# Kernel optimization log

Measured on AMD Instinct MI355X. Metric: run time of the kernel, lower is better.

Reference implementation:

```python
import jax, jax.numpy as jnp
import numpy as np
from jax import lax

MAX_INT = 10000.0
V, T0, E, H = 100000, 20, 256, 256
T = T0 + 2          # tagset_size + 2 (start = T-2, stop = T-1)
B, S = 32, 512
H2 = H // 2


def setup_inputs() -> dict:
    key = jax.random.key(0)
    ks = jax.random.split(key, 18)
    sd = 0.08
    trans = jax.random.normal(ks[0], (T, T), jnp.float32)
    trans = trans.at[-2, :].set(-MAX_INT).at[:, -1].set(-MAX_INT)
    return {
        "X": jax.random.randint(ks[1], (B, S), 0, V, jnp.int64),
        "Y": jax.random.randint(ks[2], (B, S), 0, T0, jnp.int64),
        "emb": jax.random.normal(ks[3], (V, E), jnp.float32) * sd,
        "Wih_f": jax.random.normal(ks[4], (4 * H2, E), jnp.float32) * sd,
        "Whh_f": jax.random.normal(ks[5], (4 * H2, H2), jnp.float32) * sd,
        "bih_f": jax.random.normal(ks[6], (4 * H2,), jnp.float32) * sd,
        "bhh_f": jax.random.normal(ks[7], (4 * H2,), jnp.float32) * sd,
        "Wih_b": jax.random.normal(ks[8], (4 * H2, E), jnp.float32) * sd,
        "Whh_b": jax.random.normal(ks[9], (4 * H2, H2), jnp.float32) * sd,
        "bih_b": jax.random.normal(ks[10], (4 * H2,), jnp.float32) * sd,
        "bhh_b": jax.random.normal(ks[11], (4 * H2,), jnp.float32) * sd,
        "fcW": jax.random.normal(ks[12], (T, H), jnp.float32) * sd,
        "fcb": jax.random.normal(ks[13], (T,), jnp.float32) * sd,
        "trans": trans,
        # original draws random (h0, c0) of shape (2, seq_len, H//2) each call
        "h0": jax.random.normal(ks[14], (2, S, H2), jnp.float32),
        "c0": jax.random.normal(ks[15], (2, S, H2), jnp.float32),
    }


def _lstm_dir(x, h0, c0, Wih, Whh, bih, bhh, reverse):
    # x: [B, S, E]; scans over axis 0 (as torch LSTM with batch_first=False does here)
    def step(carry, xt):
        h, c = carry
        g = xt @ Wih.T + bih + h @ Whh.T + bhh          # [S, 4*H2]
        i, f, gg, o = jnp.split(g, 4, axis=-1)
        c2 = jax.nn.sigmoid(f) * c + jax.nn.sigmoid(i) * jnp.tanh(gg)
        h2 = jax.nn.sigmoid(o) * jnp.tanh(c2)
        return (h2, c2), h2
    xs = x[::-1] if reverse else x
    _, hs = lax.scan(step, (h0, c0), xs)
    return hs[::-1] if reverse else hs                  # [B, S, H2]


def _feats(X, emb, Wih_f, Whh_f, bih_f, bhh_f, Wih_b, Whh_b, bih_b, bhh_b,
           fcW, fcb, h0, c0):
    e = emb[X]                                           # [B, S, E]
    hf = _lstm_dir(e, h0[0], c0[0], Wih_f, Whh_f, bih_f, bhh_f, False)
    hb = _lstm_dir(e, h0[1], c0[1], Wih_b, Whh_b, bih_b, bhh_b, True)
    lstm_out = jnp.concatenate([hf, hb], axis=-1)        # [B, S, H]
    return lstm_out @ fcW.T + fcb                        # [B, S, T]


def _crf_loss(feats, Y, trans):
    # forward algorithm (log partition), vectorized over batch
    alpha0 = jnp.full((B, T), -MAX_INT, feats.dtype).at[:, -2].set(0.0)

    def step(alpha, feat_t):                             # feat_t: [B, T]
        # alpha_new[b, next] = LSE_prev(alpha[b,prev] + trans[next,prev]) + feat[b,next]
        new = jax.nn.logsumexp(alpha[:, None, :] + trans[None, :, :], axis=2) + feat_t
        return new, None

    alpha, _ = lax.scan(step, alpha0, jnp.swapaxes(feats, 0, 1))
    forward_score = jax.nn.logsumexp(alpha + trans[-1][None, :], axis=1).mean()

    # gold score
    start = jnp.full((B, 1), T - 2, Y.dtype)
    tags = jnp.concatenate([start, Y], axis=1)           # [B, S+1]
    emit = jnp.take_along_axis(feats, Y[..., None], axis=2)[..., 0].sum(axis=1)
    trans_sc = trans[tags[:, 1:], tags[:, :-1]].sum(axis=1) + trans[-1, tags[:, -1]]
    gold_score = (emit + trans_sc).mean()
    return forward_score - gold_score


def reference(X, Y, emb, Wih_f, Whh_f, bih_f, bhh_f, Wih_b, Whh_b, bih_b, bhh_b,
              fcW, fcb, trans, h0, c0):
    feats = _feats(X, emb, Wih_f, Whh_f, bih_f, bhh_f, Wih_b, Whh_b, bih_b, bhh_b,
                   fcW, fcb, h0, c0)
    score = _crf_loss(feats, Y, trans)
    return score, Y
```

## Files before the change

kernel.cpp:

```cpp
#include <hip/hip_runtime.h>
#include <hip/hip_bf16.h>
#include <stdint.h>

typedef __attribute__((ext_vector_type(8))) short short8;
typedef __attribute__((ext_vector_type(4))) float f32x4;
typedef __attribute__((ext_vector_type(4))) unsigned short ushort4v;

#define NB 32
#define NS 512
#define NE 256
#define NH2 128
#define NG 512
#define NT 22

__device__ __forceinline__ unsigned short f2bf(float f) {
    union { float f; unsigned u; } v; v.f = f;
    unsigned r = v.u + 0x7fffu + ((v.u >> 16) & 1u);
    return (unsigned short)(r >> 16);
}
__device__ __forceinline__ float bf2f(unsigned short b) {
    union { unsigned u; float f; } v; v.u = ((unsigned)b) << 16;
    return v.f;
}
__device__ __forceinline__ float sigmoidf_(float x) {
    return __builtin_amdgcn_rcpf(1.f + __expf(-x));
}
__device__ __forceinline__ float tanhf_(float x) {
    return 1.f - 2.f * __builtin_amdgcn_rcpf(__expf(2.f * x) + 1.f);
}
__device__ __forceinline__ void wg_barrier() {
    __builtin_amdgcn_sched_barrier(0);
    asm volatile("s_waitcnt lgkmcnt(0)" ::: "memory");
    __builtin_amdgcn_s_barrier();
    __builtin_amdgcn_sched_barrier(0);
}
#define GL16(gsrc, ldst)                                                              \
    __builtin_amdgcn_global_load_lds(                                                 \
        (const __attribute__((address_space(1))) unsigned int*)(gsrc),                \
        (__attribute__((address_space(3))) unsigned int*)(ldst), 16, 0, 0)

__global__ void k_prep(const float* Wih_f, const float* Wih_b,
                       const float* Whh_f, const float* Whh_b,
                       const float* fcW,
                       unsigned short* Wb_ih, unsigned short* Wb_hh,
                       unsigned short* fcpad)
{
    int idx = blockIdx.x * blockDim.x + threadIdx.x;
    const int n1 = 2 * NG * NE;
    const int n2 = 2 * NG * NH2;
    const int n3 = 2 * 32 * NH2;
    if (idx < n1) {
        const float* src = (idx < NG * NE) ? Wih_f : Wih_b;
        Wb_ih[idx] = f2bf(src[idx % (NG * NE)]);
    } else if (idx < n1 + n2) {
        int i2 = idx - n1;
        const float* src = (i2 < NG * NH2) ? Whh_f : Whh_b;
        Wb_hh[i2] = f2bf(src[i2 % (NG * NH2)]);
    } else if (idx < n1 + n2 + n3) {
        int i3 = idx - n1 - n2;
        int d = i3 / (32 * NH2);
        int j = (i3 / NH2) % 32;
        int k = i3 % NH2;
        fcpad[i3] = (j < NT) ? f2bf(fcW[j * 256 + d * NH2 + k]) : (unsigned short)0;
    }
}

__global__ void k_embcvt(const int* X, const float* emb, unsigned short* ebf)
{
    int r = blockIdx.x * 4 + (threadIdx.x >> 6);
    int lane = threadIdx.x & 63;
    int xr = X[r];
    f32x4 v = *(const f32x4*)(emb + (size_t)xr * NE + lane * 4);
    ushort4v o;
    o[0] = f2bf(v[0]); o[1] = f2bf(v[1]); o[2] = f2bf(v[2]); o[3] = f2bf(v[3]);
    *(ushort4v*)(ebf + (size_t)r * NE + lane * 4) = o;
}

__launch_bounds__(256)
__global__ void k_xproj(const unsigned short* ebf, const unsigned short* Wb_ih,
                        const float* bih_f, const float* bhh_f,
                        const float* bih_b, const float* bhh_b,
                        unsigned short* Xp)
{
    __shared__ __align__(16) unsigned short Atile[128 * 64];
    __shared__ __align__(16) unsigned short Btile[128 * 64];
    int dir = blockIdx.z;
    int r0 = blockIdx.x * 128;
    int g0 = blockIdx.y * 128;
    int tid = threadIdx.x;
    int w = tid >> 6, lane = tid & 63;
    int wr = w >> 1, wc = w & 1;
    int lrow = lane & 15, kg = lane >> 4;
    int srow8 = lane >> 3, schunk = lane & 7;
    const float* bih = dir ? bih_b : bih_f;
    const float* bhh = dir ? bhh_b : bhh_f;
    const unsigned short* Bsrc = Wb_ih + ((size_t)dir * NG + g0) * NE;
    const unsigned short* Asrc = ebf + (size_t)r0 * NE;

    f32x4 acc[4][4] = {};
#pragma unroll
    for (int ks = 0; ks < 4; ++ks) {
        int k0 = ks * 64;
#pragma unroll
        for (int i = 0; i < 4; ++i) {
            int rr = (w * 4 + i) * 8 + srow8;
            GL16(Asrc + (size_t)rr * NE + k0 + schunk * 8, Atile + (w * 4 + i) * 512);
            GL16(Bsrc + (size_t)rr * NE + k0 + schunk * 8, Btile + (w * 4 + i) * 512);
        }
        __syncthreads();
        short8 a[4][2], b[4][2];
#pragma unroll
        for (int mi = 0; mi < 4; ++mi)
#pragma unroll
            for (int kk = 0; kk < 2; ++kk)
                a[mi][kk] = *(const short8*)&Atile[(wr * 64 + mi * 16 + lrow) * 64 + kk * 32 + kg * 8];
#pragma unroll
        for (int ni = 0; ni < 4; ++ni)
#pragma unroll
            for (int kk = 0; kk < 2; ++kk)
                b[ni][kk] = *(const short8*)&Btile[(wc * 64 + ni * 16 + lrow) * 64 + kk * 32 + kg * 8];
#pragma unroll
        for (int mi = 0; mi < 4; ++mi)
#pragma unroll
            for (int ni = 0; ni < 4; ++ni)
#pragma unroll
                for (int kk = 0; kk < 2; ++kk)
                    acc[mi][ni] = __builtin_amdgcn_mfma_f32_16x16x32_bf16(a[mi][kk], b[ni][kk], acc[mi][ni], 0, 0, 0);
        __syncthreads();
    }

#pragma unroll
    for (int ni = 0; ni < 4; ++ni) {
        int g = g0 + wc * 64 + ni * 16 + lrow;
        float bias = bih[g] + bhh[g];
#pragma unroll
        for (int mi = 0; mi < 4; ++mi) {
            int r = r0 + wr * 64 + mi * 16 + kg * 4;
            int t = r >> 9;
            int s = r & 511;
            int sb = s >> 4;
            unsigned short* dst = Xp + ((((size_t)dir * 32 + sb) * 32 + t) << 13) + g * 16 + (s & 15);
            unsigned o0 = f2bf(acc[mi][ni][0] + bias);
            unsigned o1 = f2bf(acc[mi][ni][1] + bias);
            unsigned o2 = f2bf(acc[mi][ni][2] + bias);
            unsigned o3 = f2bf(acc[mi][ni][3] + bias);
            uint2 pk; pk.x = o0 | (o1 << 16); pk.y = o2 | (o3 << 16);
            *(uint2*)dst = pk;
        }
    }
}

__launch_bounds__(512, 2)
__global__ void k_lstm(const unsigned short* Wb_hh, unsigned short* Xp,
                       const float* h0, const float* c0)
{
    __shared__ unsigned short h_lds[16 * 136];
    __shared__ float gates_lds[16 * 516];
    int dir = blockIdx.x >> 5;
    int sb = blockIdx.x & 31;
    int s0 = sb * 16;
    int tid = threadIdx.x;
    int w = tid >> 6, lane = tid & 63;
    int lrow = lane & 15, kg = lane >> 4;
    int sl = tid >> 5, hq = tid & 31;

    short8 bfr[4][4];
#pragma unroll
    for (int nf = 0; nf < 4; ++nf) {
        const unsigned short* p = Wb_hh + ((size_t)dir * NG + (w * 64 + nf * 16 + lrow)) * NH2 + kg * 8;
#pragma unroll
        for (int kf = 0; kf < 4; ++kf)
            bfr[nf][kf] = *(const short8*)(p + kf * 32);
    }

    float c[4];
    {
        f32x4 cv = *(const f32x4*)(c0 + ((size_t)dir * NS + s0 + sl) * NH2 + hq * 4);
        c[0] = cv[0]; c[1] = cv[1]; c[2] = cv[2]; c[3] = cv[3];
        f32x4 hv = *(const f32x4*)(h0 + ((size_t)dir * NS + s0 + sl) * NH2 + hq * 4);
        ushort4v hb; hb[0] = f2bf(hv[0]); hb[1] = f2bf(hv[1]); hb[2] = f2bf(hv[2]); hb[3] = f2bf(hv[3]);
        *(ushort4v*)&h_lds[sl * 136 + hq * 4] = hb;
    }

    unsigned short* xslot0 = Xp + (((size_t)dir * 32 + sb) * 32) * 8192;
    const unsigned short* xlane = xslot0 + (w * 64 + lrow) * 16 + kg * 4;
    int tx0 = dir ? 31 : 0;
    ushort4v xv[4], xvn[4];
#pragma unroll
    for (int nf = 0; nf < 4; ++nf)
        xv[nf] = *(const ushort4v*)(xlane + (size_t)tx0 * 8192 + nf * 256);
    __syncthreads();

    for (int t = 0; t < 32; ++t) {
        int tx  = dir ? 31 - t : t;
        int txn = dir ? 30 - t : t + 1;
        if (t < 31) {
#pragma unroll
            for (int nf = 0; nf < 4; ++nf)
                xvn[nf] = *(const ushort4v*)(xlane + (size_t)txn * 8192 + nf * 256);
        }
        short8 afr[4];
#pragma unroll
        for (int kf = 0; kf < 4; ++kf)
            afr[kf] = *(const short8*)&h_lds[lrow * 136 + kf * 32 + kg * 8];
        f32x4 acc[4] = {};
#pragma unroll
        for (int nf = 0; nf < 4; ++nf)
#pragma unroll
            for (int kf = 0; kf < 4; ++kf)
                acc[nf] = __builtin_amdgcn_mfma_f32_16x16x32_bf16(afr[kf], bfr[nf][kf], acc[nf], 0, 0, 0);
#pragma unroll
        for (int nf = 0; nf < 4; ++nf) {
            int g = w * 64 + nf * 16 + lrow;
#pragma unroll
            for (int i = 0; i < 4; ++i)
                gates_lds[(kg * 4 + i) * 516 + g] = acc[nf][i] + bf2f(xv[nf][i]);
        }
        wg_barrier();
        {
            const float* gl = gates_lds + sl * 516 + hq * 4;
            f32x4 gi = *(const f32x4*)(gl);
            f32x4 gf = *(const f32x4*)(gl + 128);
            f32x4 gg = *(const f32x4*)(gl + 256);
            f32x4 go = *(const f32x4*)(gl + 384);
            ushort4v hb;
#pragma unroll
            for (int e = 0; e < 4; ++e) {
                float ci = sigmoidf_(gf[e]) * c[e] + sigmoidf_(gi[e]) * tanhf_(gg[e]);
                c[e] = ci;
                hb[e] = f2bf(sigmoidf_(go[e]) * tanhf_(ci));
            }
            *(ushort4v*)&h_lds[sl * 136 + hq * 4] = hb;
            *(ushort4v*)(xslot0 + (size_t)tx * 8192 + sl * 128 + hq * 4) = hb;
        }
        wg_barrier();
#pragma unroll
        for (int nf = 0; nf < 4; ++nf) xv[nf] = xvn[nf];
    }
}

__launch_bounds__(128)
__global__ void k_fc(const unsigned short* Hout, const unsigned short* fcpad,
                     const float* fcb, float* feats)
{
    __shared__ f32x4 part[2][64];
    int t = blockIdx.x, sb = blockIdx.y;
    int tid = threadIdx.x;
    int dir = tid >> 6, lane = tid & 63;
    int lrow = lane & 15, kg = lane >> 4;
    const unsigned short* hb = Hout + ((((size_t)dir * 32 + sb) * 32 + t) << 13) + lrow * 128 + kg * 8;
    const unsigned short* fb = fcpad + dir * 4096 + lrow * 128 + kg * 8;
    f32x4 acc[2] = {};
#pragma unroll
    for (int kf = 0; kf < 4; ++kf) {
        short8 a  = *(const short8*)(hb + kf * 32);
        short8 b0 = *(const short8*)(fb + kf * 32);
        short8 b1 = *(const short8*)(fb + 2048 + kf * 32);
        acc[0] = __builtin_amdgcn_mfma_f32_16x16x32_bf16(a, b0, acc[0], 0, 0, 0);
        acc[1] = __builtin_amdgcn_mfma_f32_16x16x32_bf16(a, b1, acc[1], 0, 0, 0);
    }
    if (dir == 1) { part[0][lane] = acc[0]; part[1][lane] = acc[1]; }
    __syncthreads();
    if (dir == 0) {
        acc[0] += part[0][lane];
        acc[1] += part[1][lane];
#pragma unroll
        for (int nf = 0; nf < 2; ++nf) {
            int tag = nf * 16 + lrow;
            if (tag < NT) {
                float bias = fcb[tag];
#pragma unroll
                for (int i = 0; i < 4; ++i)
                    feats[((size_t)t * NS + sb * 16 + kg * 4 + i) * NT + tag] = acc[nf][i] + bias;
            }
        }
    }
}

__device__ __forceinline__ float mm_combine(const unsigned short* Rb, const unsigned short* Tb,
                                            int lane, f32x4 c[2][2])
{
    int lrow = lane & 15, kg = lane >> 4;
    short8 a0 = *(const short8*)(Rb + lrow * 32 + kg * 8);
    short8 a1 = *(const short8*)(Rb + (16 + lrow) * 32 + kg * 8);
    short8 b0 = *(const short8*)(Tb + lrow * 32 + kg * 8);
    short8 b1 = *(const short8*)(Tb + (16 + lrow) * 32 + kg * 8);
    c[0][0] = __builtin_amdgcn_mfma_f32_16x16x32_bf16(a0, b0, c[0][0], 0, 0, 0);
    c[0][1] = __builtin_amdgcn_mfma_f32_16x16x32_bf16(a0, b1, c[0][1], 0, 0, 0);
    c[1][0] = __builtin_amdgcn_mfma_f32_16x16x32_bf16(a1, b0, c[1][0], 0, 0, 0);
    c[1][1] = __builtin_amdgcn_mfma_f32_16x16x32_bf16(a1, b1, c[1][1], 0, 0, 0);
    float mx = 0.f;
#pragma unroll
    for (int ti = 0; ti < 2; ++ti)
#pragma unroll
        for (int tj = 0; tj < 2; ++tj)
#pragma unroll
            for (int i = 0; i < 4; ++i) mx = fmaxf(mx, c[ti][tj][i]);
#pragma unroll
    for (int off = 32; off; off >>= 1) mx = fmaxf(mx, __shfl_xor(mx, off));
    return fmaxf(mx, 1e-30f);
}

__device__ __forceinline__ void write_scaled(unsigned short* outp, bool Rlayout,
                                             int lane, const f32x4 c[2][2], float inv)
{
    int lrow = lane & 15, kg = lane >> 4;
    if (Rlayout) {
#pragma unroll
        for (int ti = 0; ti < 2; ++ti)
#pragma unroll
            for (int tj = 0; tj < 2; ++tj) {
                int cc = tj * 16 + lrow;
#pragma unroll
                for (int i = 0; i < 4; ++i) {
                    int r = ti * 16 + kg * 4 + i;
                    float v = (r < NT && cc < NT) ? c[ti][tj][i] * inv : 0.f;
                    outp[r * 32 + cc] = f2bf(v);
                }
            }
    } else {
#pragma unroll
        for (int ti = 0; ti < 2; ++ti)
#pragma unroll
            for (int tj = 0; tj < 2; ++tj) {
                int cc = tj * 16 + lrow;
                int r0 = ti * 16 + kg * 4;
                ushort4v pk;
#pragma unroll
                for (int i = 0; i < 4; ++i) {
                    int r = r0 + i;
                    float v = (r < NT && cc < NT) ? c[ti][tj][i] * inv : 0.f;
                    pk[i] = f2bf(v);
                }
                *(ushort4v*)(outp + cc * 32 + r0) = pk;
            }
    }
}

__launch_bounds__(256)
__global__ void k_crf1(const float* feats, const float* trans,
                       unsigned short* Mseg, float* lscseg)
{
    __shared__ unsigned short mats[16 * 1024];
    __shared__ float etR[484], etT[484];
    __shared__ float ef[16 * 24];
    __shared__ float lscm[16];
    int seg = blockIdx.x, b = blockIdx.y;
    int tid = threadIdx.x;
    int w = tid >> 6, lane = tid & 63;

    for (int i = tid; i < 484; i += 256) {
        float e = __expf(trans[i]);
        etR[i] = e;
        etT[(i % NT) * NT + (i / NT)] = e;
    }
    for (int i = tid; i < 16 * NT; i += 256) {
        int t = i / NT, j = i % NT;
        ef[t * 24 + j] = __expf(feats[((size_t)b * NS + seg * 16 + t) * NT + j]);
    }
    if (tid < 16) lscm[tid] = 0.f;
    __syncthreads();

    for (int idx = tid; idx < 16 * 1024; idx += 256) {
        int t = idx >> 10, cell = idx & 1023, row = cell >> 5, col = cell & 31;
        float v = 0.f;
        if (row < NT && col < NT) {
            v = (t & 1) ? etR[row * NT + col] * ef[t * 24 + row]
                        : etT[row * NT + col] * ef[t * 24 + col];
        }
        mats[idx] = f2bf(v);
    }
    __syncthreads();

    for (int lvl = 0; lvl < 4; ++lvl) {
        int nP = 8 >> lvl;
        for (int p = w; p < nP; p += 4) {
            int aslot = (2 * p) << lvl, bslot = (2 * p + 1) << lvl;
            f32x4 c[2][2] = {};
            float mx = mm_combine(mats + bslot * 1024, mats + aslot * 1024, lane, c);
            float inv = __builtin_amdgcn_rcpf(mx);
            float nlsc = lscm[aslot] + lscm[bslot] + __logf(mx);
            if (lvl < 3) {
                write_scaled(mats + aslot * 1024, (p & 1) != 0, lane, c, inv);
                if (lane == 0) lscm[aslot] = nlsc;
            } else {
                write_scaled(Mseg + ((size_t)b * 32 + seg) * 1024, (seg & 1) != 0, lane, c, inv);
                if (lane == 0) lscseg[b * 32 + seg] = nlsc;
            }
        }
        __syncthreads();
    }
}

__launch_bounds__(256)
__global__ void k_crf2(const unsigned short* Mseg, const float* lscseg,
                       const float* feats, const float* trans, const int* Y,
                       float* fwd_sc, float* gold_sc)
{
    __shared__ unsigned short mats[16 * 1024];
    __shared__ float lscm[16];
    __shared__ float tl[484];
    __shared__ float col20[32];
    __shared__ float red[4];
    int b = blockIdx.x;
    int tid = threadIdx.x;
    int w = tid >> 6, lane = tid & 63;
    int lrow = lane & 15, kg = lane >> 4;

    for (int i = tid; i < 484; i += 256) tl[i] = trans[i];
    __syncthreads();

    const unsigned short* base = Mseg + (size_t)b * 32 * 1024;
    for (int p = w; p < 16; p += 4) {
        f32x4 c[2][2] = {};
        float mx = mm_combine(base + (2 * p + 1) * 1024, base + (2 * p) * 1024, lane, c);
        float inv = __builtin_amdgcn_rcpf(mx);
        float nlsc = lscseg[b * 32 + 2 * p] + lscseg[b * 32 + 2 * p + 1] + __logf(mx);
        write_scaled(mats + p * 1024, (p & 1) != 0, lane, c, inv);
        if (lane == 0) lscm[p] = nlsc;
    }
    __syncthreads();

    for (int lvl = 0; lvl < 4; ++lvl) {
        int nP = 8 >> lvl;
        for (int p = w; p < nP; p += 4) {
            int aslot = (2 * p) << lvl, bslot = (2 * p + 1) << lvl;
            f32x4 c[2][2] = {};
            float mx = mm_combine(mats + bslot * 1024, mats + aslot * 1024, lane, c);
            if (lvl < 3) {
                float inv = __builtin_amdgcn_rcpf(mx);
                float nlsc = lscm[aslot] + lscm[bslot] + __logf(mx);
                write_scaled(mats + aslot * 1024, (p & 1) != 0, lane, c, inv);
                if (lane == 0) lscm[aslot] = nlsc;
            } else {
                if (lrow == 4) {
#pragma unroll
                    for (int ti = 0; ti < 2; ++ti)
#pragma unroll
                        for (int i = 0; i < 4; ++i)
                            col20[ti * 16 + kg * 4 + i] = c[ti][1][i];
                }
                if (lane == 0) lscm[0] = lscm[0] + lscm[8];
            }
        }
        __syncthreads();
    }

    if (w == 0) {
        float v = 0.f;
        if (lane < NT) v = __expf(tl[(NT - 1) * NT + lane]) * col20[lane];
#pragma unroll
        for (int off = 32; off; off >>= 1) v += __shfl_xor(v, off);
        if (lane == 0) fwd_sc[b] = __logf(v) + lscm[0];
    }

    const float* fb = feats + (size_t)b * NS * NT;
    float acc = 0.f;
    for (int s = tid; s < NS; s += 256) {
        int y = Y[b * NS + s];
        int yp = s ? Y[b * NS + s - 1] : (NT - 2);
        acc += fb[s * NT + y] + tl[y * NT + yp];
    }
    if (tid == 0) acc += tl[(NT - 1) * NT + Y[b * NS + NS - 1]];
#pragma unroll
    for (int off = 32; off; off >>= 1) acc += __shfl_xor(acc, off);
    if (lane == 0) red[w] = acc;
    __syncthreads();
    if (tid == 0) gold_sc[b] = red[0] + red[1] + red[2] + red[3];
}

__global__ void k_final(const float* fwd_sc, const float* gold_sc, const int* Y, float* out)
{
    int idx = blockIdx.x * blockDim.x + threadIdx.x;
    if (blockIdx.x == 0 && threadIdx.x < 64) {
        float v = (threadIdx.x < NB) ? (fwd_sc[threadIdx.x] - gold_sc[threadIdx.x]) : 0.f;
#pragma unroll
        for (int off = 32; off; off >>= 1) v += __shfl_xor(v, off);
        if (threadIdx.x == 0) out[0] = v * (1.f / NB);
    }
    if (idx < NB * NS) out[1 + idx] = (float)Y[idx];
}

extern "C" void kernel_launch(void* const* d_in, const int* in_sizes, int n_in,
                              void* d_out, int out_size, void* d_ws, size_t ws_size,
                              hipStream_t stream)
{
    const int* X = (const int*)d_in[0];
    const int* Y = (const int*)d_in[1];
    const float* emb = (const float*)d_in[2];
    const float* Wih_f = (const float*)d_in[3];
    const float* Whh_f = (const float*)d_in[4];
    const float* bih_f = (const float*)d_in[5];
    const float* bhh_f = (const float*)d_in[6];
    const float* Wih_b = (const float*)d_in[7];
    const float* Whh_b = (const float*)d_in[8];
    const float* bih_b = (const float*)d_in[9];
    const float* bhh_b = (const float*)d_in[10];
    const float* fcW = (const float*)d_in[11];
    const float* fcb = (const float*)d_in[12];
    const float* trans = (const float*)d_in[13];
    const float* h0 = (const float*)d_in[14];
    const float* c0 = (const float*)d_in[15];
    float* out = (float*)d_out;

    char* ws = (char*)d_ws;
    unsigned short* Wb_ih = (unsigned short*)(ws + 0);
    unsigned short* Wb_hh = (unsigned short*)(ws + 524288);
    unsigned short* fcpad = (unsigned short*)(ws + 786432);
    unsigned short* Xp    = (unsigned short*)(ws + 802816);
    float* feats          = (float*)(ws + 34357248);
    float* fwd_sc         = (float*)(ws + 35799040);
    float* gold_sc        = (float*)(ws + 35799168);
    unsigned short* ebf   = (unsigned short*)(ws + 35799296);
    unsigned short* Mseg  = ebf;
    float* lscseg         = (float*)(ws + 35799296 + 2097152);

    k_prep<<<dim3(1568), dim3(256), 0, stream>>>(Wih_f, Wih_b, Whh_f, Whh_b, fcW,
                                                 Wb_ih, Wb_hh, fcpad);
    k_embcvt<<<dim3(4096), dim3(256), 0, stream>>>(X, emb, ebf);
    k_xproj<<<dim3(128, 4, 2), dim3(256), 0, stream>>>(ebf, Wb_ih, bih_f, bhh_f, bih_b, bhh_b, Xp);
    k_lstm<<<dim3(64), dim3(512), 0, stream>>>(Wb_hh, Xp, h0, c0);
    k_fc<<<dim3(32, 32), dim3(128), 0, stream>>>(Xp, fcpad, fcb, feats);
    k_crf1<<<dim3(32, 32), dim3(256), 0, stream>>>(feats, trans, Mseg, lscseg);
    k_crf2<<<dim3(NB), dim3(256), 0, stream>>>(Mseg, lscseg, feats, trans, Y, fwd_sc, gold_sc);
    k_final<<<dim3(64), dim3(256), 0, stream>>>(fwd_sc, gold_sc, Y, out);
    (void)in_sizes; (void)n_in; (void)out_size; (void)ws_size;
}
```

Baseline: 110.0 us.

## Fuse prep kernels, restructure LSTM step to register gates, fuse FC into CRF

Merges embedding conversion, weight conversion and the Y copy-out into one prep kernel. The LSTM step is remapped so that each lane keeps all four gates for its own hidden units in registers. This removes the gates LDS round trip and one barrier per step, and it double-buffers h in LDS and prefetches x two steps ahead. The FC projection is fused into the CRF segment kernel, which saves a launch and a feats reload. The cost is more register pressure in the LSTM and an extra Hout workspace buffer.

```diff
diff --git a/kernel.cpp b/kernel.cpp
--- a/kernel.cpp
+++ b/kernel.cpp
@@ -39,41 +39,45 @@
         (const __attribute__((address_space(1))) unsigned int*)(gsrc),                \
         (__attribute__((address_space(3))) unsigned int*)(ldst), 16, 0, 0)
 
-__global__ void k_prep(const float* Wih_f, const float* Wih_b,
-                       const float* Whh_f, const float* Whh_b,
-                       const float* fcW,
-                       unsigned short* Wb_ih, unsigned short* Wb_hh,
-                       unsigned short* fcpad)
+__global__ void k_pre(const int* X, const float* emb, const int* Y,
+                      const float* Wih_f, const float* Wih_b,
+                      const float* Whh_f, const float* Whh_b, const float* fcW,
+                      unsigned short* ebf, unsigned short* Wb_ih,
+                      unsigned short* Wb_hh, unsigned short* fcpad, float* out)
 {
     int idx = blockIdx.x * blockDim.x + threadIdx.x;
+    const int nEmb = NB * NS * 64;
+    if (idx < nEmb) {
+        int r = idx >> 6, lane = idx & 63;
+        int xr = X[r];
+        f32x4 v = *(const f32x4*)(emb + (size_t)xr * NE + lane * 4);
+        ushort4v o;
+        o[0] = f2bf(v[0]); o[1] = f2bf(v[1]); o[2] = f2bf(v[2]); o[3] = f2bf(v[3]);
+        *(ushort4v*)(ebf + (size_t)r * NE + lane * 4) = o;
+        return;
+    }
+    int j = idx - nEmb;
     const int n1 = 2 * NG * NE;
     const int n2 = 2 * NG * NH2;
     const int n3 = 2 * 32 * NH2;
-    if (idx < n1) {
-        const float* src = (idx < NG * NE) ? Wih_f : Wih_b;
-        Wb_ih[idx] = f2bf(src[idx % (NG * NE)]);
-    } else if (idx < n1 + n2) {
-        int i2 = idx - n1;
+    const int n4 = NB * NS;
+    if (j < n1) {
+        const float* src = (j < NG * NE) ? Wih_f : Wih_b;
+        Wb_ih[j] = f2bf(src[j % (NG * NE)]);
+    } else if (j < n1 + n2) {
+        int i2 = j - n1;
         const float* src = (i2 < NG * NH2) ? Whh_f : Whh_b;
         Wb_hh[i2] = f2bf(src[i2 % (NG * NH2)]);
-    } else if (idx < n1 + n2 + n3) {
-        int i3 = idx - n1 - n2;
+    } else if (j < n1 + n2 + n3) {
+        int i3 = j - n1 - n2;
         int d = i3 / (32 * NH2);
-        int j = (i3 / NH2) % 32;
+        int jj = (i3 / NH2) % 32;
         int k = i3 % NH2;
-        fcpad[i3] = (j < NT) ? f2bf(fcW[j * 256 + d * NH2 + k]) : (unsigned short)0;
-    }
-}
-
-__global__ void k_embcvt(const int* X, const float* emb, unsigned short* ebf)
-{
-    int r = blockIdx.x * 4 + (threadIdx.x >> 6);
-    int lane = threadIdx.x & 63;
-    int xr = X[r];
-    f32x4 v = *(const f32x4*)(emb + (size_t)xr * NE + lane * 4);
-    ushort4v o;
-    o[0] = f2bf(v[0]); o[1] = f2bf(v[1]); o[2] = f2bf(v[2]); o[3] = f2bf(v[3]);
-    *(ushort4v*)(ebf + (size_t)r * NE + lane * 4) = o;
+        fcpad[i3] = (jj < NT) ? f2bf(fcW[jj * 256 + d * NH2 + k]) : (unsigned short)0;
+    } else if (j < n1 + n2 + n3 + n4) {
+        int i4 = j - n1 - n2 - n3;
+        out[1 + i4] = (float)Y[i4];
+    }
 }
 
 __launch_bounds__(256)
@@ -151,130 +155,92 @@
 }
 
 __launch_bounds__(512, 2)
-__global__ void k_lstm(const unsigned short* Wb_hh, unsigned short* Xp,
-                       const float* h0, const float* c0)
-{
-    __shared__ unsigned short h_lds[16 * 136];
-    __shared__ float gates_lds[16 * 516];
+__global__ void k_lstm(const unsigned short* Wb_hh, const unsigned short* Xp,
+                       unsigned short* Hout, const float* h0, const float* c0)
+{
+    __shared__ unsigned short h_lds[2][16 * 136];
     int dir = blockIdx.x >> 5;
     int sb = blockIdx.x & 31;
     int s0 = sb * 16;
     int tid = threadIdx.x;
     int w = tid >> 6, lane = tid & 63;
     int lrow = lane & 15, kg = lane >> 4;
-    int sl = tid >> 5, hq = tid & 31;
 
     short8 bfr[4][4];
 #pragma unroll
-    for (int nf = 0; nf < 4; ++nf) {
-        const unsigned short* p = Wb_hh + ((size_t)dir * NG + (w * 64 + nf * 16 + lrow)) * NH2 + kg * 8;
+    for (int q = 0; q < 4; ++q) {
+        const unsigned short* p = Wb_hh + ((size_t)dir * NG + (q * 128 + w * 16 + lrow)) * NH2 + kg * 8;
 #pragma unroll
         for (int kf = 0; kf < 4; ++kf)
-            bfr[nf][kf] = *(const short8*)(p + kf * 32);
+            bfr[q][kf] = *(const short8*)(p + kf * 32);
     }
 
     float c[4];
+#pragma unroll
+    for (int i = 0; i < 4; ++i)
+        c[i] = c0[((size_t)dir * NS + s0 + kg * 4 + i) * NH2 + w * 16 + lrow];
     {
-        f32x4 cv = *(const f32x4*)(c0 + ((size_t)dir * NS + s0 + sl) * NH2 + hq * 4);
-        c[0] = cv[0]; c[1] = cv[1]; c[2] = cv[2]; c[3] = cv[3];
+        int sl = tid >> 5, hq = tid & 31;
         f32x4 hv = *(const f32x4*)(h0 + ((size_t)dir * NS + s0 + sl) * NH2 + hq * 4);
         ushort4v hb; hb[0] = f2bf(hv[0]); hb[1] = f2bf(hv[1]); hb[2] = f2bf(hv[2]); hb[3] = f2bf(hv[3]);
-        *(ushort4v*)&h_lds[sl * 136 + hq * 4] = hb;
-    }
-
-    unsigned short* xslot0 = Xp + (((size_t)dir * 32 + sb) * 32) * 8192;
-    const unsigned short* xlane = xslot0 + (w * 64 + lrow) * 16 + kg * 4;
-    int tx0 = dir ? 31 : 0;
-    ushort4v xv[4], xvn[4];
-#pragma unroll
-    for (int nf = 0; nf < 4; ++nf)
-        xv[nf] = *(const ushort4v*)(xlane + (size_t)tx0 * 8192 + nf * 256);
-    __syncthreads();
-
-    for (int t = 0; t < 32; ++t) {
-        int tx  = dir ? 31 - t : t;
-        int txn = dir ? 30 - t : t + 1;
-        if (t < 31) {
-#pragma unroll
-            for (int nf = 0; nf < 4; ++nf)
-                xvn[nf] = *(const ushort4v*)(xlane + (size_t)txn * 8192 + nf * 256);
-        }
-        short8 afr[4];
-#pragma unroll
-        for (int kf = 0; kf < 4; ++kf)
-            afr[kf] = *(const short8*)&h_lds[lrow * 136 + kf * 32 + kg * 8];
-        f32x4 acc[4] = {};
-#pragma unroll
-        for (int nf = 0; nf < 4; ++nf)
-#pragma unroll
-            for (int kf = 0; kf < 4; ++kf)
-                acc[nf] = __builtin_amdgcn_mfma_f32_16x16x32_bf16(afr[kf], bfr[nf][kf], acc[nf], 0, 0, 0);
-#pragma unroll
-        for (int nf = 0; nf < 4; ++nf) {
-            int g = w * 64 + nf * 16 + lrow;
-#pragma unroll
-            for (int i = 0; i < 4; ++i)
-                gates_lds[(kg * 4 + i) * 516 + g] = acc[nf][i] + bf2f(xv[nf][i]);
-        }
-        wg_barrier();
-        {
-            const float* gl = gates_lds + sl * 516 + hq * 4;
-            f32x4 gi = *(const f32x4*)(gl);
-            f32x4 gf = *(const f32x4*)(gl + 128);
-            f32x4 gg = *(const f32x4*)(gl + 256);
-            f32x4 go = *(const f32x4*)(gl + 384);
-            ushort4v hb;
-#pragma unroll
-            for (int e = 0; e < 4; ++e) {
-                float ci = sigmoidf_(gf[e]) * c[e] + sigmoidf_(gi[e]) * tanhf_(gg[e]);
-                c[e] = ci;
-                hb[e] = f2bf(sigmoidf_(go[e]) * tanhf_(ci));
-            }
-            *(ushort4v*)&h_lds[sl * 136 + hq * 4] = hb;
-            *(ushort4v*)(xslot0 + (size_t)tx * 8192 + sl * 128 + hq * 4) = hb;
-        }
-        wg_barrier();
-#pragma unroll
-        for (int nf = 0; nf < 4; ++nf) xv[nf] = xvn[nf];
-    }
-}
-
-__launch_bounds__(128)
-__global__ void k_fc(const unsigned short* Hout, const unsigned short* fcpad,
-                     const float* fcb, float* feats)
-{
-    __shared__ f32x4 part[2][64];
-    int t = blockIdx.x, sb = blockIdx.y;
-    int tid = threadIdx.x;
-    int dir = tid >> 6, lane = tid & 63;
-    int lrow = lane & 15, kg = lane >> 4;
-    const unsigned short* hb = Hout + ((((size_t)dir * 32 + sb) * 32 + t) << 13) + lrow * 128 + kg * 8;
-    const unsigned short* fb = fcpad + dir * 4096 + lrow * 128 + kg * 8;
-    f32x4 acc[2] = {};
-#pragma unroll
-    for (int kf = 0; kf < 4; ++kf) {
-        short8 a  = *(const short8*)(hb + kf * 32);
-        short8 b0 = *(const short8*)(fb + kf * 32);
-        short8 b1 = *(const short8*)(fb + 2048 + kf * 32);
-        acc[0] = __builtin_amdgcn_mfma_f32_16x16x32_bf16(a, b0, acc[0], 0, 0, 0);
-        acc[1] = __builtin_amdgcn_mfma_f32_16x16x32_bf16(a, b1, acc[1], 0, 0, 0);
-    }
-    if (dir == 1) { part[0][lane] = acc[0]; part[1][lane] = acc[1]; }
-    __syncthreads();
-    if (dir == 0) {
-        acc[0] += part[0][lane];
-        acc[1] += part[1][lane];
-#pragma unroll
-        for (int nf = 0; nf < 2; ++nf) {
-            int tag = nf * 16 + lrow;
-            if (tag < NT) {
-                float bias = fcb[tag];
-#pragma unroll
-                for (int i = 0; i < 4; ++i)
-                    feats[((size_t)t * NS + sb * 16 + kg * 4 + i) * NT + tag] = acc[nf][i] + bias;
-            }
-        }
-    }
+        *(ushort4v*)&h_lds[0][sl * 136 + hq * 4] = hb;
+    }
+
+    const unsigned short* xbase = Xp + (((size_t)dir * 32 + sb) * 32) * 8192;
+    unsigned short* hslot = Hout + (((size_t)dir * 32 + sb) * 32) * 2048;
+    int xoff0 = (w * 16 + lrow) * 16 + kg * 4;
+
+    ushort4v xA[4], xB[4];
+#pragma unroll
+    for (int q = 0; q < 4; ++q)
+        xA[q] = *(const ushort4v*)(xbase + (size_t)(dir ? 31 : 0) * 8192 + xoff0 + q * 2048);
+#pragma unroll
+    for (int q = 0; q < 4; ++q)
+        xB[q] = *(const ushort4v*)(xbase + (size_t)(dir ? 30 : 1) * 8192 + xoff0 + q * 2048);
+    __syncthreads();
+
+#define LSTM_STEP(T, XV, PR, PW)                                                       \
+    {                                                                                  \
+        int tx = dir ? 31 - (T) : (T);                                                 \
+        short8 afr[4];                                                                 \
+        _Pragma("unroll")                                                              \
+        for (int kf = 0; kf < 4; ++kf)                                                 \
+            afr[kf] = *(const short8*)&h_lds[PR][lrow * 136 + kf * 32 + kg * 8];       \
+        f32x4 acc[4] = {};                                                             \
+        _Pragma("unroll")                                                              \
+        for (int q = 0; q < 4; ++q)                                                    \
+            _Pragma("unroll")                                                          \
+            for (int kf = 0; kf < 4; ++kf)                                             \
+                acc[q] = __builtin_amdgcn_mfma_f32_16x16x32_bf16(afr[kf], bfr[q][kf],  \
+                                                                 acc[q], 0, 0, 0);     \
+        float gs[4][4];                                                                \
+        _Pragma("unroll")                                                              \
+        for (int q = 0; q < 4; ++q)                                                    \
+            _Pragma("unroll")                                                          \
+            for (int i = 0; i < 4; ++i)                                                \
+                gs[q][i] = acc[q][i] + bf2f(XV[q][i]);                                 \
+        if ((T) + 2 < 32) {                                                            \
+            int txn = dir ? 29 - (T) : (T) + 2;                                        \
+            _Pragma("unroll")                                                          \
+            for (int q = 0; q < 4; ++q)                                                \
+                XV[q] = *(const ushort4v*)(xbase + (size_t)txn * 8192 + xoff0 + q * 2048); \
+        }                                                                              \
+        _Pragma("unroll")                                                              \
+        for (int i = 0; i < 4; ++i) {                                                  \
+            float ci = sigmoidf_(gs[1][i]) * c[i] + sigmoidf_(gs[0][i]) * tanhf_(gs[2][i]); \
+            c[i] = ci;                                                                 \
+            unsigned short hb = f2bf(sigmoidf_(gs[3][i]) * tanhf_(ci));                \
+            h_lds[PW][(kg * 4 + i) * 136 + w * 16 + lrow] = hb;                        \
+            hslot[(size_t)tx * 2048 + (kg * 4 + i) * 128 + w * 16 + lrow] = hb;        \
+        }                                                                              \
+        wg_barrier();                                                                  \
+    }
+
+    for (int tt = 0; tt < 16; ++tt) {
+        LSTM_STEP(2 * tt,     xA, ((2 * tt) & 1),     (((2 * tt) & 1) ^ 1))
+        LSTM_STEP(2 * tt + 1, xB, ((2 * tt + 1) & 1), (((2 * tt + 1) & 1) ^ 1))
+    }
+#undef LSTM_STEP
 }
 
 __device__ __forceinline__ float mm_combine(const unsigned short* Rb, const unsigned short* Tb,
@@ -338,27 +304,61 @@
 }
 
 __launch_bounds__(256)
-__global__ void k_crf1(const float* feats, const float* trans,
-                       unsigned short* Mseg, float* lscseg)
+__global__ void k_fcrf(const unsigned short* Hout, const unsigned short* fcpad,
+                       const float* fcb, const float* trans,
+                       float* feats, unsigned short* Mseg, float* lscseg)
 {
     __shared__ unsigned short mats[16 * 1024];
     __shared__ float etR[484], etT[484];
     __shared__ float ef[16 * 24];
     __shared__ float lscm[16];
-    int seg = blockIdx.x, b = blockIdx.y;
+    __shared__ f32x4 part[2][64];
+    int b = blockIdx.x, seg = blockIdx.y;
     int tid = threadIdx.x;
     int w = tid >> 6, lane = tid & 63;
-
-    for (int i = tid; i < 484; i += 256) {
-        float e = __expf(trans[i]);
-        etR[i] = e;
-        etT[(i % NT) * NT + (i / NT)] = e;
-    }
-    for (int i = tid; i < 16 * NT; i += 256) {
-        int t = i / NT, j = i % NT;
-        ef[t * 24 + j] = __expf(feats[((size_t)b * NS + seg * 16 + t) * NT + j]);
-    }
-    if (tid < 16) lscm[tid] = 0.f;
+    int lrow = lane & 15, kg = lane >> 4;
+
+    f32x4 fa[2] = {};
+    if (w < 2) {
+        int dir = w;
+        const unsigned short* hb = Hout + (((size_t)dir * 32 + seg) * 32 + b) * 2048 + lrow * 128 + kg * 8;
+        const unsigned short* fb = fcpad + dir * 4096 + lrow * 128 + kg * 8;
+#pragma unroll
+        for (int kf = 0; kf < 4; ++kf) {
+            short8 a  = *(const short8*)(hb + kf * 32);
+            short8 b0 = *(const short8*)(fb + kf * 32);
+            short8 b1 = *(const short8*)(fb + 2048 + kf * 32);
+            fa[0] = __builtin_amdgcn_mfma_f32_16x16x32_bf16(a, b0, fa[0], 0, 0, 0);
+            fa[1] = __builtin_amdgcn_mfma_f32_16x16x32_bf16(a, b1, fa[1], 0, 0, 0);
+        }
+        if (dir == 1) { part[0][lane] = fa[0]; part[1][lane] = fa[1]; }
+        if (w == 1 && lane < 16) lscm[lane] = 0.f;
+    } else {
+        for (int i = tid - 128; i < 484; i += 128) {
+            float e = __expf(trans[i]);
+            etR[i] = e;
+            etT[(i % NT) * NT + (i / NT)] = e;
+        }
+    }
+    __syncthreads();
+    if (w == 0) {
+        fa[0] += part[0][lane];
+        fa[1] += part[1][lane];
+#pragma unroll
+        for (int nf = 0; nf < 2; ++nf) {
+            int tag = nf * 16 + lrow;
+            if (tag < NT) {
+                float bias = fcb[tag];
+#pragma unroll
+                for (int i = 0; i < 4; ++i) {
+                    int s = kg * 4 + i;
+                    float f = fa[nf][i] + bias;
+                    feats[((size_t)b * NS + seg * 16 + s) * NT + tag] = f;
+                    ef[s * 24 + tag] = __expf(f);
+                }
+            }
+        }
+    }
     __syncthreads();
 
     for (int idx = tid; idx < 16 * 1024; idx += 256) {
@@ -469,16 +469,12 @@
     if (tid == 0) gold_sc[b] = red[0] + red[1] + red[2] + red[3];
 }
 
-__global__ void k_final(const float* fwd_sc, const float* gold_sc, const int* Y, float* out)
-{
-    int idx = blockIdx.x * blockDim.x + threadIdx.x;
-    if (blockIdx.x == 0 && threadIdx.x < 64) {
-        float v = (threadIdx.x < NB) ? (fwd_sc[threadIdx.x] - gold_sc[threadIdx.x]) : 0.f;
-#pragma unroll
-        for (int off = 32; off; off >>= 1) v += __shfl_xor(v, off);
-        if (threadIdx.x == 0) out[0] = v * (1.f / NB);
-    }
-    if (idx < NB * NS) out[1 + idx] = (float)Y[idx];
+__global__ void k_final(const float* fwd_sc, const float* gold_sc, float* out)
+{
+    float v = (threadIdx.x < NB) ? (fwd_sc[threadIdx.x] - gold_sc[threadIdx.x]) : 0.f;
+#pragma unroll
+    for (int off = 32; off; off >>= 1) v += __shfl_xor(v, off);
+    if (threadIdx.x == 0) out[0] = v * (1.f / NB);
 }
 
 extern "C" void kernel_launch(void* const* d_in, const int* in_sizes, int n_in,
@@ -514,15 +510,14 @@
     unsigned short* ebf   = (unsigned short*)(ws + 35799296);
     unsigned short* Mseg  = ebf;
     float* lscseg         = (float*)(ws + 35799296 + 2097152);
-
-    k_prep<<<dim3(1568), dim3(256), 0, stream>>>(Wih_f, Wih_b, Whh_f, Whh_b, fcW,
-                                                 Wb_ih, Wb_hh, fcpad);
-    k_embcvt<<<dim3(4096), dim3(256), 0, stream>>>(X, emb, ebf);
+    unsigned short* Hout  = (unsigned short*)(ws + 44187904);
+
+    k_pre<<<dim3(5728), dim3(256), 0, stream>>>(X, emb, Y, Wih_f, Wih_b, Whh_f, Whh_b,
+                                                fcW, ebf, Wb_ih, Wb_hh, fcpad, out);
     k_xproj<<<dim3(128, 4, 2), dim3(256), 0, stream>>>(ebf, Wb_ih, bih_f, bhh_f, bih_b, bhh_b, Xp);
-    k_lstm<<<dim3(64), dim3(512), 0, stream>>>(Wb_hh, Xp, h0, c0);
-    k_fc<<<dim3(32, 32), dim3(128), 0, stream>>>(Xp, fcpad, fcb, feats);
-    k_crf1<<<dim3(32, 32), dim3(256), 0, stream>>>(feats, trans, Mseg, lscseg);
+    k_lstm<<<dim3(64), dim3(512), 0, stream>>>(Wb_hh, Xp, Hout, h0, c0);
+    k_fcrf<<<dim3(32, 32), dim3(256), 0, stream>>>(Hout, fcpad, fcb, trans, feats, Mseg, lscseg);
     k_crf2<<<dim3(NB), dim3(256), 0, stream>>>(Mseg, lscseg, feats, trans, Y, fwd_sc, gold_sc);
-    k_final<<<dim3(64), dim3(256), 0, stream>>>(fwd_sc, gold_sc, Y, out);
+    k_final<<<dim3(1), dim3(64), 0, stream>>>(fwd_sc, gold_sc, out);
     (void)in_sizes; (void)n_in; (void)out_size; (void)ws_size;
 }
```

Measured after the change: 97.65 us. 11.2% less time.
